# Kernel tuning notes

Measured on AMD Instinct MI355X. Metric: run time of the kernel, lower is better.

## Reference

```python
import jax, jax.numpy as jnp
import numpy as np

N_NODES = 50000
N_EDGES = 800000
IN_FEATS = 128
OUT_FEATS = 128
FREQ_DIM = OUT_FEATS // 2 + 1
BN_EPS = 1e-5


def setup_inputs() -> dict:
    key = jax.random.key(0)
    ks = jax.random.split(key, 8)
    x = jax.random.normal(ks[0], (N_NODES, IN_FEATS), dtype=jnp.float32)
    edge_index = jax.random.randint(ks[1], (2, N_EDGES), 0, N_NODES, dtype=jnp.int64)
    # lin_fusion: Linear(2*in_feats, out_feats)
    W_fuse = jax.random.normal(ks[2], (OUT_FEATS, 2 * IN_FEATS), dtype=jnp.float32) * (1.0 / np.sqrt(2 * IN_FEATS))
    b_fuse = jnp.zeros((OUT_FEATS,), dtype=jnp.float32)
    # lin_in: Linear(in_feats, out_feats)
    W_in = jax.random.normal(ks[3], (OUT_FEATS, IN_FEATS), dtype=jnp.float32) * (1.0 / np.sqrt(IN_FEATS))
    b_in = jnp.zeros((OUT_FEATS,), dtype=jnp.float32)
    complex_weight = jax.random.normal(ks[4], (FREQ_DIM, 2), dtype=jnp.float32) * 0.02
    alpha = jnp.float32(0.5)
    gamma = jnp.ones((OUT_FEATS,), dtype=jnp.float32)
    beta = jnp.zeros((OUT_FEATS,), dtype=jnp.float32)
    return {"x": x, "edge_index": edge_index, "W_fuse": W_fuse, "b_fuse": b_fuse,
            "W_in": W_in, "b_in": b_in, "complex_weight": complex_weight,
            "alpha": alpha, "gamma": gamma, "beta": beta}


def reference(x, edge_index, W_fuse, b_fuse, W_in, b_in, complex_weight, alpha, gamma, beta):
    N = x.shape[0]
    src, dst = edge_index[0], edge_index[1]
    # --- spatial branch: scatter-mean aggregation of neighbor features ---
    msgs = x[src]  # [E, in] gather
    agg_sum = jax.ops.segment_sum(msgs, dst, num_segments=N)  # [N, in]
    cnt = jax.ops.segment_sum(jnp.ones((src.shape[0],), dtype=x.dtype), dst, num_segments=N)
    aggs = agg_sum / jnp.maximum(cnt, 1.0)[:, None]
    combined = jnp.concatenate([x, aggs], axis=1)  # [N, 2*in]
    x_spatial = combined @ W_fuse.T + b_fuse  # [N, out]
    # --- spectral branch: linear -> rfft * complex weight -> irfft ---
    h = x @ W_in.T + b_in  # [N, out]
    hf = jnp.fft.rfft(h, axis=-1)  # [N, out//2+1]
    w = complex_weight[:, 0] + 1j * complex_weight[:, 1]
    x_spectral = jnp.fft.irfft(hf * w, n=h.shape[-1], axis=-1).astype(x.dtype)
    # --- fuse + BatchNorm1d (training stats, biased var) + exact GELU ---
    out = x_spatial + alpha * x_spectral
    mean = jnp.mean(out, axis=0)
    var = jnp.mean(jnp.square(out - mean), axis=0)
    out = (out - mean) / jnp.sqrt(var + BN_EPS) * gamma + beta
    return jax.nn.gelu(out, approximate=False)
```

## Files before the change

### kernel.cpp

```cpp
#include <hip/hip_runtime.h>
#include <hip/hip_bf16.h>

#define NN 50000
#define NE 800000
#define FD 128
#define FREQ 65
#define CAP 64
#define BN_EPS 1e-5f

#define NB_CVT  6250
#define NB_WCB  128
#define NGRP 8
#define GRPN 6250
#define NCHUNK 256
#define CHUNKE 3125
#define NB_BKT (NGRP * NCHUNK)
#define SENT NN

typedef unsigned int u32;
typedef unsigned short u16;
typedef __attribute__((ext_vector_type(8))) short short8;
typedef __attribute__((ext_vector_type(4))) float float4v;
typedef __attribute__((ext_vector_type(2))) float floatx2;

__device__ __forceinline__ float bf2f(u16 v) {
    return __uint_as_float(((u32)v) << 16);
}
__device__ __forceinline__ u16 f2bf(float f) {
    u32 u = __float_as_uint(f);
    u32 lsb = (u >> 16) & 1u;
    return (u16)((u + 0x7fffu + lsb) >> 16);
}
__device__ __forceinline__ float ldf(const void* p, int i, int f32) {
    return f32 ? ((const float*)p)[i] : bf2f(((const u16*)p)[i]);
}
__device__ __forceinline__ int detect_f32(const void* gamma) {
    return ((const u32*)gamma)[0] == 0x3F800000u;
}
__device__ __forceinline__ int detect_idx64(const int* idx) {
    return (idx[1] | idx[3] | idx[5] | idx[7] |
            idx[9] | idx[11] | idx[13] | idx[15]) == 0;
}

__device__ __forceinline__ u32 pk4_e4m3(float a, float b, float c, float d) {
#if __has_builtin(__builtin_amdgcn_cvt_pk_fp8_f32)
    int r = __builtin_amdgcn_cvt_pk_fp8_f32(a, b, 0, false);
    r = __builtin_amdgcn_cvt_pk_fp8_f32(c, d, r, true);
    return (u32)r;
#else
    auto one = [](float f) -> u32 {
        u32 u = __float_as_uint(f);
        u32 s = (u >> 24) & 0x80u;
        float af = fabsf(f);
        if (af > 448.f) return s | 0x7Eu;
        if (af < 7.8125e-3f) return s;
        int e = (int)((u >> 23) & 255) - 127;
        u32 m = (u >> 20) & 7u;
        u32 rnd = (u >> 19) & 1u;
        u32 sticky = (u & 0x7FFFFu) ? 1u : 0u;
        m += (rnd & (sticky | (m & 1u)));
        u32 ee = (u32)(e + 7);
        if (m > 7u) { m = 0u; ee += 1u; }
        if (ee > 15u) return s | 0x7Eu;
        return s | (ee << 3) | m;
    };
    return one(a) | (one(b) << 8) | (one(c) << 16) | (one(d) << 24);
#endif
}
__device__ __forceinline__ void deq4_e4m3(u32 p, float& a, float& b, float& c, float& d) {
#if __has_builtin(__builtin_amdgcn_cvt_pk_f32_fp8)
    floatx2 lo = __builtin_amdgcn_cvt_pk_f32_fp8((int)p, false);
    floatx2 hi = __builtin_amdgcn_cvt_pk_f32_fp8((int)p, true);
    a = lo.x; b = lo.y; c = hi.x; d = hi.y;
#else
    auto one = [](u32 v) -> float {
        u32 s = (v & 0x80u) << 24;
        u32 e = (v >> 3) & 15u;
        u32 m = v & 7u;
        if (e == 0) {
            float f = (float)m * 0.001953125f;
            return s ? -f : f;
        }
        return __uint_as_float(s | ((e + 120u) << 23) | (m << 20));
    };
    a = one(p & 255u); b = one((p >> 8) & 255u);
    c = one((p >> 16) & 255u); d = one(p >> 24);
#endif
}

#define WS_WCB       0
#define WS_BIAS      65536
#define WS_X8        66048
#define WS_ZSTART    6466048
#define WS_BNSUM     6466176
#define WS_BNSQ      6466688
#define WS_DEG       6467200
#define WS_ZEND      6667200
#define WS_CSR16     6667200
#define WS_AGG16     13067200
#define WS_OUT16     25867200

__global__ __launch_bounds__(256) void prep_kernel(const void* __restrict__ x,
                                                   const int* __restrict__ idx,
                                                   const void* __restrict__ Wf,
                                                   const void* __restrict__ bfu,
                                                   const void* __restrict__ Wi,
                                                   const void* __restrict__ bi,
                                                   const void* __restrict__ cw,
                                                   const void* __restrict__ alpha_p,
                                                   const void* __restrict__ gamma,
                                                   u32* __restrict__ x8,
                                                   u16* __restrict__ WcB,
                                                   float* __restrict__ bias,
                                                   int* __restrict__ deg,
                                                   u16* __restrict__ csr) {
    int b = blockIdx.x;
    int t = threadIdx.x;
    if (b < NB_CVT) {
        int gid = b * 256 + t;
        float a, bb, c, d;
        if (detect_f32(gamma)) {
            float4 v = ((const float4*)x)[gid];
            a = v.x; bb = v.y; c = v.z; d = v.w;
        } else {
            uint2 v = ((const uint2*)x)[gid];
            a = bf2f((u16)(v.x & 0xffffu)); bb = bf2f((u16)(v.x >> 16));
            c = bf2f((u16)(v.y & 0xffffu)); d = bf2f((u16)(v.y >> 16));
        }
        x8[gid] = pk4_e4m3(a, bb, c, d);
        return;
    }
    b -= NB_CVT;
    if (b >= NB_WCB) {
        int b2 = b - NB_WCB;
        int g = b2 & (NGRP - 1);
        int chunk = b2 >> 3;
        int lo = g * GRPN, hi = lo + GRPN;
        int base = chunk * CHUNKE;
        int i64f = detect_idx64(idx);
        for (int i = t; i < CHUNKE; i += 256) {
            int e = base + i;
            int src, dst;
            if (i64f) { src = idx[2 * e]; dst = idx[2 * NE + 2 * e]; }
            else      { src = idx[e];     dst = idx[NE + e]; }
            if (dst >= lo && dst < hi) {
                int pos = atomicAdd(deg + dst, 1);
                if (pos < CAP) csr[(size_t)dst * CAP + pos] = (u16)src;
            }
        }
        return;
    }
    int f32 = detect_f32(gamma);
    int j = b;
    __shared__ float wr[FREQ], wi[FREQ];
    __shared__ float cl[128];
    __shared__ float part[256];
    if (t < FREQ) { wr[t] = ldf(cw, 2 * t, f32); wi[t] = ldf(cw, 2 * t + 1, f32); }
    __syncthreads();
    if (t < 128) {
        float s = wr[0] + ((t & 1) ? -wr[64] : wr[64]);
        for (int f = 1; f < 64; ++f) {
            int ph = (f * t) & 127;
            float th = (float)ph * (6.283185307179586f / 128.f);
            float sn, cs;
            sincosf(th, &sn, &cs);
            s += 2.f * (wr[f] * cs - wi[f] * sn);
        }
        cl[t] = s * (1.f / 128.f);
    }
    __syncthreads();
    int k = t & 127, mh = t >> 7;
    float acc = 0.f;
    int m0 = mh * 64;
#pragma unroll 8
    for (int mm = 0; mm < 64; ++mm) {
        int m = m0 + mm;
        acc = fmaf(ldf(Wi, m * 128 + k, f32), cl[(j - m) & 127], acc);
    }
    part[t] = acc;
    __syncthreads();
    if (t < 128) {
        float al = ldf(alpha_p, 0, f32);
        int ct = j >> 4;
        float v = ldf(Wf, j * 256 + k, f32) + al * (part[k] + part[k + 128]);
        int off = (((ct * 8 + (k >> 5)) * 64) + ((k >> 3) & 3) * 16 + (j & 15)) * 8 + (k & 7);
        WcB[off] = f2bf(v);
        int k2 = k + 128;
        float v2 = ldf(Wf, j * 256 + k2, f32);
        int off2 = (((ct * 8 + (k2 >> 5)) * 64) + ((k2 >> 3) & 3) * 16 + (j & 15)) * 8 + (k2 & 7);
        WcB[off2] = f2bf(v2);
        if (j == 0) {
            float bacc = 0.f;
            for (int m = 0; m < 128; ++m)
                bacc = fmaf(ldf(bi, m, f32), cl[(t - m) & 127], bacc);
            bias[t] = ldf(bfu, t, f32) + al * bacc;
        }
    }
}

__global__ __launch_bounds__(256) void aggregate_kernel(const u32* __restrict__ x8,
                                                        const u16* __restrict__ csr,
                                                        const int* __restrict__ deg,
                                                        u32* __restrict__ agg16) {
    int gid = blockIdx.x * 256 + threadIdx.x;
    int n = gid >> 6;
    int lane = threadIdx.x & 63;
    if (n >= NN) return;
    int q = lane & 31;
    int h = lane >> 5;
    const u32* csrw = (const u32*)csr;
    int dc = deg[n];
    int cnt = min(dc, CAP);
    u32 cv = csrw[(size_t)n * (CAP / 2) + q];
    u32 e0 = (2 * q     < cnt) ? (cv & 0xffffu) : (u32)SENT;
    u32 e1 = (2 * q + 1 < cnt) ? (cv >> 16)     : (u32)SENT;
    cv = e0 | (e1 << 16);

    float a0 = 0.f, a1 = 0.f, a2 = 0.f, a3 = 0.f;
    for (int jj = 0; jj < cnt; jj += 16) {
        u32 p[8];
#pragma unroll
        for (int r = 0; r < 8; ++r) {
            int i = jj + 2 * r + h;
            u32 w = __shfl(cv, i >> 1);
            u32 s = (i & 1) ? (w >> 16) : (w & 0xffffu);
            p[r] = x8[(size_t)s * 32 + q];
        }
#pragma unroll
        for (int r = 0; r < 8; ++r) {
            float b0, b1, b2, b3;
            deq4_e4m3(p[r], b0, b1, b2, b3);
            a0 += b0; a1 += b1; a2 += b2; a3 += b3;
        }
    }
    a0 += __shfl_xor(a0, 32); a1 += __shfl_xor(a1, 32);
    a2 += __shfl_xor(a2, 32); a3 += __shfl_xor(a3, 32);
    if (h == 0) {
        float rinv = 1.f / fmaxf((float)dc, 1.f);
        uint2 w;
        w.x = (u32)f2bf(a0 * rinv) | ((u32)f2bf(a1 * rinv) << 16);
        w.y = (u32)f2bf(a2 * rinv) | ((u32)f2bf(a3 * rinv) << 16);
        ((uint2*)agg16)[(size_t)n * 32 + q] = w;
    }
}

__global__ __launch_bounds__(256) void gemm_kernel(const void* __restrict__ x,
                                                   const u16* __restrict__ agg16,
                                                   const void* __restrict__ gamma,
                                                   const u16* __restrict__ WcB,
                                                   const float* __restrict__ bias,
                                                   u16* __restrict__ outp16,
                                                   float* __restrict__ bnsum,
                                                   float* __restrict__ bnsq) {
    __shared__ float lsum[FD], lsq[FD];
    int t = threadIdx.x;
    if (t < FD) { lsum[t] = 0.f; lsq[t] = 0.f; }
    __syncthreads();
    int f32 = detect_f32(gamma);
    int wave = t >> 6;
    int lane = t & 63;
    int quad = lane >> 4;
    int lm = lane & 15;
    int n0 = blockIdx.x * 64;
    int nrow = n0 + wave * 16 + lm;
    bool avalid = (nrow < NN);

    float4v acc[8];
#pragma unroll
    for (int ct = 0; ct < 8; ++ct) acc[ct] = (float4v){0.f, 0.f, 0.f, 0.f};

    const short8* bp = (const short8*)WcB;
#pragma unroll
    for (int ks = 0; ks < 8; ++ks) {
        short8 a = (short8)0;
        if (avalid) {
            if (ks < 4) {
                int k = ks * 32 + quad * 8;
                if (f32) {
                    const float4* p = (const float4*)x + (size_t)nrow * 32 + (k >> 2);
                    float4 v0 = p[0], v1 = p[1];
                    a[0] = (short)f2bf(v0.x); a[1] = (short)f2bf(v0.y);
                    a[2] = (short)f2bf(v0.z); a[3] = (short)f2bf(v0.w);
                    a[4] = (short)f2bf(v1.x); a[5] = (short)f2bf(v1.y);
                    a[6] = (short)f2bf(v1.z); a[7] = (short)f2bf(v1.w);
                } else {
                    a = ((const short8*)x)[(size_t)nrow * 16 + (k >> 3)];
                }
            } else {
                int k = (ks - 4) * 32 + quad * 8;
                a = ((const short8*)agg16)[(size_t)nrow * 16 + (k >> 3)];
            }
        }
#pragma unroll
        for (int ct = 0; ct < 8; ++ct) {
            short8 b = bp[(ct * 8 + ks) * 64 + lane];
            acc[ct] = __builtin_amdgcn_mfma_f32_16x16x32_bf16(a, b, acc[ct], 0, 0, 0);
        }
    }

    int rbase = n0 + wave * 16 + quad * 4;
#pragma unroll
    for (int ct = 0; ct < 8; ++ct) {
        int col = ct * 16 + lm;
        float bj = bias[col];
        float s = 0.f, q = 0.f;
#pragma unroll
        for (int r = 0; r < 4; ++r) {
            int n = rbase + r;
            if (n < NN) {
                float v = acc[ct][r] + bj;
                outp16[(size_t)n * FD + col] = f2bf(v);
                s += v;
                q = fmaf(v, v, q);
            }
        }
        s += __shfl_xor(s, 16); s += __shfl_xor(s, 32);
        q += __shfl_xor(q, 16); q += __shfl_xor(q, 32);
        if (lane < 16) {
            atomicAdd(&lsum[col], s);
            atomicAdd(&lsq[col], q);
        }
    }
    __syncthreads();
    if (t < FD) {
        atomicAdd(bnsum + t, lsum[t]);
        atomicAdd(bnsq + t, lsq[t]);
    }
}

__global__ __launch_bounds__(256) void apply_kernel(const u32* __restrict__ outp16,
                                                    const float* __restrict__ bnsum,
                                                    const float* __restrict__ bnsq,
                                                    const void* __restrict__ gamma,
                                                    const void* __restrict__ beta,
                                                    void* __restrict__ out) {
    __shared__ float sc[FD], sh[FD];
    int t = threadIdx.x;
    int f32 = detect_f32(gamma);
    if (t < FD) {
        float mean = bnsum[t] * (1.f / NN);
        float var = bnsq[t] * (1.f / NN) - mean * mean;
        float s = ldf(gamma, t, f32) / sqrtf(var + BN_EPS);
        sc[t] = s;
        sh[t] = ldf(beta, t, f32) - mean * s;
    }
    __syncthreads();
    int gid = blockIdx.x * 256 + t;
    if (gid >= NN * (FD / 8)) return;
    uint4 pk = ((const uint4*)outp16)[gid];
    int f0 = (gid * 8) & 127;
    u32 w[4] = {pk.x, pk.y, pk.z, pk.w};
    float g[8];
#pragma unroll
    for (int q = 0; q < 4; ++q) {
        float v0 = bf2f((u16)(w[q] & 0xffffu));
        float v1 = bf2f((u16)(w[q] >> 16));
        float z0 = fmaf(v0, sc[f0 + 2 * q], sh[f0 + 2 * q]);
        float z1 = fmaf(v1, sc[f0 + 2 * q + 1], sh[f0 + 2 * q + 1]);
        g[2 * q]     = 0.5f * z0 * (1.f + erff(z0 * 0.70710678118654752f));
        g[2 * q + 1] = 0.5f * z1 * (1.f + erff(z1 * 0.70710678118654752f));
    }
    if (f32) {
        float4* o = (float4*)out + (size_t)gid * 2;
        o[0] = make_float4(g[0], g[1], g[2], g[3]);
        o[1] = make_float4(g[4], g[5], g[6], g[7]);
    } else {
        uint4 o;
        o.x = (u32)f2bf(g[0]) | ((u32)f2bf(g[1]) << 16);
        o.y = (u32)f2bf(g[2]) | ((u32)f2bf(g[3]) << 16);
        o.z = (u32)f2bf(g[4]) | ((u32)f2bf(g[5]) << 16);
        o.w = (u32)f2bf(g[6]) | ((u32)f2bf(g[7]) << 16);
        ((uint4*)out)[gid] = o;
    }
}

extern "C" void kernel_launch(void* const* d_in, const int* in_sizes, int n_in,
                              void* d_out, int out_size, void* d_ws, size_t ws_size,
                              hipStream_t stream) {
    const void* x     = d_in[0];
    const int* eidx   = (const int*)d_in[1];
    const void* Wf    = d_in[2];
    const void* bfu   = d_in[3];
    const void* Wi    = d_in[4];
    const void* bi    = d_in[5];
    const void* cw    = d_in[6];
    const void* alpha = d_in[7];
    const void* gamma = d_in[8];
    const void* beta  = d_in[9];

    char* ws = (char*)d_ws;
    u16*   WcB    = (u16*)(ws + WS_WCB);
    float* bias   = (float*)(ws + WS_BIAS);
    u32*   x8     = (u32*)(ws + WS_X8);
    float* bnsum  = (float*)(ws + WS_BNSUM);
    float* bnsq   = (float*)(ws + WS_BNSQ);
    int*   deg    = (int*)(ws + WS_DEG);
    u16*   csr    = (u16*)(ws + WS_CSR16);
    u32*   agg16  = (u32*)(ws + WS_AGG16);
    u16*   outp16 = (u16*)(ws + WS_OUT16);

    hipMemsetAsync(ws + WS_ZSTART, 0, (size_t)WS_ZEND - WS_ZSTART, stream);

    prep_kernel<<<NB_CVT + NB_WCB + NB_BKT, 256, 0, stream>>>(
        x, eidx, Wf, bfu, Wi, bi, cw, alpha, gamma, x8, WcB, bias, deg, csr);
    aggregate_kernel<<<(NN * 64 + 255) / 256, 256, 0, stream>>>(x8, csr, deg, agg16);
    gemm_kernel<<<(NN + 63) / 64, 256, 0, stream>>>(x, (const u16*)agg16, gamma, WcB,
                                                    bias, outp16, bnsum, bnsq);
    apply_kernel<<<(NN * (FD / 8) + 255) / 256, 256, 0, stream>>>((const u32*)outp16,
                                                                  bnsum, bnsq, gamma,
                                                                  beta, d_out);
}
```

Baseline: 206.9 us.

## Fuse BatchNorm+GELU apply into GEMM via grid-wide barrier and reorder prep blocks

Removes the separate apply kernel. Each GEMM block keeps its tile in registers, adds its column statistics, then spins on a global done-counter until every block has finished. It then applies BatchNorm and exact GELU and writes the final output directly. This skips the bf16 intermediate output's round trip through global memory and one kernel launch. The trade-off is that all 782 blocks must be co-resident, which launch_bounds(256,4) is meant to ensure; otherwise the spin wait would deadlock. The edge-bucketing blocks now come first in prep with smaller chunks, and src is only loaded when dst falls in the group.

```diff
diff --git a/kernel.cpp b/kernel.cpp
--- a/kernel.cpp
+++ b/kernel.cpp
@@ -12,10 +12,11 @@
 #define NB_WCB  128
 #define NGRP 8
 #define GRPN 6250
-#define NCHUNK 256
-#define CHUNKE 3125
+#define NCHUNK 800
+#define CHUNKE 1000
 #define NB_BKT (NGRP * NCHUNK)
 #define SENT NN
+#define NBLK_GEMM ((NN + 63) / 64)
 
 typedef unsigned int u32;
 typedef unsigned short u16;
@@ -94,11 +95,11 @@
 #define WS_ZSTART    6466048
 #define WS_BNSUM     6466176
 #define WS_BNSQ      6466688
-#define WS_DEG       6467200
-#define WS_ZEND      6667200
-#define WS_CSR16     6667200
-#define WS_AGG16     13067200
-#define WS_OUT16     25867200
+#define WS_CNT       6467200
+#define WS_DEG       6467264
+#define WS_ZEND      6667264
+#define WS_CSR16     6667264
+#define WS_AGG16     13067264
 
 __global__ __launch_bounds__(256) void prep_kernel(const void* __restrict__ x,
                                                    const int* __restrict__ idx,
@@ -116,6 +117,24 @@
                                                    u16* __restrict__ csr) {
     int b = blockIdx.x;
     int t = threadIdx.x;
+    if (b < NB_BKT) {
+        int g = b & (NGRP - 1);
+        int chunk = b >> 3;
+        int lo = g * GRPN, hi = lo + GRPN;
+        int base = chunk * CHUNKE;
+        int i64f = detect_idx64(idx);
+        for (int i = t; i < CHUNKE; i += 256) {
+            int e = base + i;
+            int dst = i64f ? idx[2 * NE + 2 * e] : idx[NE + e];
+            if (dst >= lo && dst < hi) {
+                int src = i64f ? idx[2 * e] : idx[e];
+                int pos = atomicAdd(deg + dst, 1);
+                if (pos < CAP) csr[(size_t)dst * CAP + pos] = (u16)src;
+            }
+        }
+        return;
+    }
+    b -= NB_BKT;
     if (b < NB_CVT) {
         int gid = b * 256 + t;
         float a, bb, c, d;
@@ -131,25 +150,6 @@
         return;
     }
     b -= NB_CVT;
-    if (b >= NB_WCB) {
-        int b2 = b - NB_WCB;
-        int g = b2 & (NGRP - 1);
-        int chunk = b2 >> 3;
-        int lo = g * GRPN, hi = lo + GRPN;
-        int base = chunk * CHUNKE;
-        int i64f = detect_idx64(idx);
-        for (int i = t; i < CHUNKE; i += 256) {
-            int e = base + i;
-            int src, dst;
-            if (i64f) { src = idx[2 * e]; dst = idx[2 * NE + 2 * e]; }
-            else      { src = idx[e];     dst = idx[NE + e]; }
-            if (dst >= lo && dst < hi) {
-                int pos = atomicAdd(deg + dst, 1);
-                if (pos < CAP) csr[(size_t)dst * CAP + pos] = (u16)src;
-            }
-        }
-        return;
-    }
     int f32 = detect_f32(gamma);
     int j = b;
     __shared__ float wr[FREQ], wi[FREQ];
@@ -244,14 +244,16 @@
     }
 }
 
-__global__ __launch_bounds__(256) void gemm_kernel(const void* __restrict__ x,
-                                                   const u16* __restrict__ agg16,
-                                                   const void* __restrict__ gamma,
-                                                   const u16* __restrict__ WcB,
-                                                   const float* __restrict__ bias,
-                                                   u16* __restrict__ outp16,
-                                                   float* __restrict__ bnsum,
-                                                   float* __restrict__ bnsq) {
+__global__ __launch_bounds__(256, 4) void gemm_kernel(const void* __restrict__ x,
+                                                      const u16* __restrict__ agg16,
+                                                      const void* __restrict__ gamma,
+                                                      const void* __restrict__ beta,
+                                                      const u16* __restrict__ WcB,
+                                                      const float* __restrict__ bias,
+                                                      float* __restrict__ bnsum,
+                                                      float* __restrict__ bnsq,
+                                                      int* __restrict__ done_cnt,
+                                                      void* __restrict__ out) {
     __shared__ float lsum[FD], lsq[FD];
     int t = threadIdx.x;
     if (t < FD) { lsum[t] = 0.f; lsq[t] = 0.f; }
@@ -306,10 +308,9 @@
         float s = 0.f, q = 0.f;
 #pragma unroll
         for (int r = 0; r < 4; ++r) {
-            int n = rbase + r;
-            if (n < NN) {
-                float v = acc[ct][r] + bj;
-                outp16[(size_t)n * FD + col] = f2bf(v);
+            float v = acc[ct][r] + bj;
+            acc[ct][r] = v;
+            if (rbase + r < NN) {
                 s += v;
                 q = fmaf(v, v, q);
             }
@@ -326,51 +327,48 @@
         atomicAdd(bnsum + t, lsum[t]);
         atomicAdd(bnsq + t, lsq[t]);
     }
-}
-
-__global__ __launch_bounds__(256) void apply_kernel(const u32* __restrict__ outp16,
-                                                    const float* __restrict__ bnsum,
-                                                    const float* __restrict__ bnsq,
-                                                    const void* __restrict__ gamma,
-                                                    const void* __restrict__ beta,
-                                                    void* __restrict__ out) {
-    __shared__ float sc[FD], sh[FD];
-    int t = threadIdx.x;
-    int f32 = detect_f32(gamma);
+    __syncthreads();
+
+    if (t == 0) {
+        __threadfence();
+        atomicAdd(done_cnt, 1);
+        while (__hip_atomic_load(done_cnt, __ATOMIC_ACQUIRE,
+                                 __HIP_MEMORY_SCOPE_AGENT) < NBLK_GEMM) {
+#if __has_builtin(__builtin_amdgcn_s_sleep)
+            __builtin_amdgcn_s_sleep(8);
+#endif
+        }
+    }
+    __syncthreads();
+
     if (t < FD) {
-        float mean = bnsum[t] * (1.f / NN);
-        float var = bnsq[t] * (1.f / NN) - mean * mean;
+        float sum = __hip_atomic_load(&bnsum[t], __ATOMIC_RELAXED,
+                                      __HIP_MEMORY_SCOPE_AGENT);
+        float sq  = __hip_atomic_load(&bnsq[t], __ATOMIC_RELAXED,
+                                      __HIP_MEMORY_SCOPE_AGENT);
+        float mean = sum * (1.f / NN);
+        float var = sq * (1.f / NN) - mean * mean;
         float s = ldf(gamma, t, f32) / sqrtf(var + BN_EPS);
-        sc[t] = s;
-        sh[t] = ldf(beta, t, f32) - mean * s;
-    }
-    __syncthreads();
-    int gid = blockIdx.x * 256 + t;
-    if (gid >= NN * (FD / 8)) return;
-    uint4 pk = ((const uint4*)outp16)[gid];
-    int f0 = (gid * 8) & 127;
-    u32 w[4] = {pk.x, pk.y, pk.z, pk.w};
-    float g[8];
-#pragma unroll
-    for (int q = 0; q < 4; ++q) {
-        float v0 = bf2f((u16)(w[q] & 0xffffu));
-        float v1 = bf2f((u16)(w[q] >> 16));
-        float z0 = fmaf(v0, sc[f0 + 2 * q], sh[f0 + 2 * q]);
-        float z1 = fmaf(v1, sc[f0 + 2 * q + 1], sh[f0 + 2 * q + 1]);
-        g[2 * q]     = 0.5f * z0 * (1.f + erff(z0 * 0.70710678118654752f));
-        g[2 * q + 1] = 0.5f * z1 * (1.f + erff(z1 * 0.70710678118654752f));
-    }
-    if (f32) {
-        float4* o = (float4*)out + (size_t)gid * 2;
-        o[0] = make_float4(g[0], g[1], g[2], g[3]);
-        o[1] = make_float4(g[4], g[5], g[6], g[7]);
-    } else {
-        uint4 o;
-        o.x = (u32)f2bf(g[0]) | ((u32)f2bf(g[1]) << 16);
-        o.y = (u32)f2bf(g[2]) | ((u32)f2bf(g[3]) << 16);
-        o.z = (u32)f2bf(g[4]) | ((u32)f2bf(g[5]) << 16);
-        o.w = (u32)f2bf(g[6]) | ((u32)f2bf(g[7]) << 16);
-        ((uint4*)out)[gid] = o;
+        lsum[t] = s;
+        lsq[t] = ldf(beta, t, f32) - mean * s;
+    }
+    __syncthreads();
+
+#pragma unroll
+    for (int ct = 0; ct < 8; ++ct) {
+        int col = ct * 16 + lm;
+        float sc = lsum[col];
+        float sh = lsq[col];
+#pragma unroll
+        for (int r = 0; r < 4; ++r) {
+            int n = rbase + r;
+            if (n < NN) {
+                float z = fmaf(acc[ct][r], sc, sh);
+                float g = 0.5f * z * (1.f + erff(z * 0.70710678118654752f));
+                if (f32) ((float*)out)[(size_t)n * FD + col] = g;
+                else     ((u16*)out)[(size_t)n * FD + col] = f2bf(g);
+            }
+        }
     }
 }
 
@@ -394,19 +392,16 @@
     u32*   x8     = (u32*)(ws + WS_X8);
     float* bnsum  = (float*)(ws + WS_BNSUM);
     float* bnsq   = (float*)(ws + WS_BNSQ);
+    int*   cnt    = (int*)(ws + WS_CNT);
     int*   deg    = (int*)(ws + WS_DEG);
     u16*   csr    = (u16*)(ws + WS_CSR16);
     u32*   agg16  = (u32*)(ws + WS_AGG16);
-    u16*   outp16 = (u16*)(ws + WS_OUT16);
 
     hipMemsetAsync(ws + WS_ZSTART, 0, (size_t)WS_ZEND - WS_ZSTART, stream);
 
-    prep_kernel<<<NB_CVT + NB_WCB + NB_BKT, 256, 0, stream>>>(
+    prep_kernel<<<NB_BKT + NB_CVT + NB_WCB, 256, 0, stream>>>(
         x, eidx, Wf, bfu, Wi, bi, cw, alpha, gamma, x8, WcB, bias, deg, csr);
     aggregate_kernel<<<(NN * 64 + 255) / 256, 256, 0, stream>>>(x8, csr, deg, agg16);
-    gemm_kernel<<<(NN + 63) / 64, 256, 0, stream>>>(x, (const u16*)agg16, gamma, WcB,
-                                                    bias, outp16, bnsum, bnsq);
-    apply_kernel<<<(NN * (FD / 8) + 255) / 256, 256, 0, stream>>>((const u32*)outp16,
-                                                                  bnsum, bnsq, gamma,
-                                                                  beta, d_out);
-}
+    gemm_kernel<<<NBLK_GEMM, 256, 0, stream>>>(x, (const u16*)agg16, gamma, beta,
+                                               WcB, bias, bnsum, bnsq, cnt, d_out);
+}
```

After: 301.1 us. +45.5%, slower.
